# Kernel optimization log

Measured on AMD Instinct MI355X. Metric: run time of the kernel, lower is better.

The kernel has to match this reference:

```python
import jax, jax.numpy as jnp
import numpy as np

K_PRED = 6
SCORE_TEMPERATURE = 0.5
NMS_THRESH = np.array([2.5, 1.0, 1.5], dtype=np.float32)  # [veh, ped, cyc] meters
SUPPRESSED_SCORE = 0.001


def setup_inputs() -> dict:
    key = jax.random.key(0)
    k0, k1, k2, k3 = jax.random.split(key, 4)
    D, S, A, P, T = 1, 64, 128, 6, 80  # n_decoder, n_scene, n_agent, n_pred, n_step_future
    pred_valid = jnp.ones((S, A), dtype=bool)
    pred_conf = jax.random.normal(k0, (D, S, A, P), dtype=jnp.float32)
    # scale positions to realistic meters so distances straddle the NMS thresholds
    pred_pos = jax.random.normal(k1, (D, S, A, P, T, 2), dtype=jnp.float32) * 10.0
    pred_yaw_bbox = jax.random.normal(k2, (D, S, A, P, T, 1), dtype=jnp.float32)
    type_idx = jax.random.randint(k3, (S, A), 0, 3)
    ref_type = jax.nn.one_hot(type_idx, 3, dtype=jnp.float32)
    return {
        'pred_valid': pred_valid,
        'pred_conf': pred_conf,
        'pred_pos': pred_pos,
        'pred_yaw_bbox': pred_yaw_bbox,
        'ref_type': ref_type,
    }


def _nms_one_agent(scores, within, valid):
    # scores: [K], within: [K, K] bool, valid: scalar bool
    order = jnp.argsort(-scores)  # descending, computed once on original scores

    def step(cur, k):
        # suppress k if any other prediction within distance has a (currently) higher score
        mask = within[k] & (cur > cur[k])
        new_val = jnp.where(jnp.any(mask), jnp.asarray(SUPPRESSED_SCORE, cur.dtype), cur[k])
        return cur.at[k].set(new_val), None

    out, _ = jax.lax.scan(step, scores, order)
    return jnp.where(valid, out, scores)


_nms = jax.vmap(jax.vmap(_nms_one_agent))  # over scene, agent


def reference(pred_valid, pred_conf, pred_pos, pred_yaw_bbox, ref_type):
    D, S, A, P, T, _ = pred_pos.shape
    K = D * P
    # [n_scene, n_agent, k_pred, n_step, 2]
    trajs = jnp.moveaxis(pred_pos, 0, 2).reshape(S, A, K, T, 2)
    scores = jax.nn.softmax(pred_conf, axis=-1)
    scores = jnp.moveaxis(scores, 0, 2).reshape(S, A, K)
    scores = scores / jnp.sum(scores, axis=-1, keepdims=True)

    # mpa_nms: per-agent-type distance threshold
    thresh = jnp.einsum('sat,t->sa', ref_type, jnp.asarray(NMS_THRESH))[:, :, None, None]
    # use_ade=True: mean pairwise distance over time -> [S, A, K, K]
    diff = trajs[:, :, :, None] - trajs[:, :, None, :]          # [S,A,K,K,T,2]
    within_dist = jnp.mean(jnp.linalg.norm(diff, axis=-1), axis=-1) < thresh
    scores = _nms(scores, within_dist, pred_valid)
    scores = scores / jnp.sum(scores, axis=-1, keepdims=True)

    # score temperature
    scores = jax.nn.softmax(jnp.log(scores) / SCORE_TEMPERATURE, axis=-1)

    waymo_trajs = jnp.moveaxis(trajs, 3, 1)                      # [S, T, A, K, 2]
    waymo_scores = scores                                        # [S, A, K]
    waymo_valid = jnp.broadcast_to(pred_valid[:, None, :], (S, T, A))
    yaw_bbox = jnp.moveaxis(pred_yaw_bbox, 0, 2).reshape(S, A, K, T, 1)
    waymo_yaw_bbox = jnp.moveaxis(yaw_bbox, 3, 1)                # [S, T, A, K, 1]
    return waymo_valid, waymo_trajs, waymo_scores, waymo_yaw_bbox
```

## Files before the change

### kernel.cpp

```cpp
#include <hip/hip_runtime.h>
#include <hip/hip_bf16.h>

#define NS 64
#define NA 128
#define NK 6
#define NT 80
#define TILE_A 8
#define THREADS 256

#define OFF_TRAJ   655360
#define OFF_SCORE  (655360 + 7864320)
#define OFF_YAW    (655360 + 7864320 + 49152)

__global__ __launch_bounds__(THREADS) void waymo_post_kernel(
    const int*    __restrict__ validIn,
    const float*  __restrict__ confIn,
    const float2* __restrict__ posIn,
    const float*  __restrict__ yawIn,
    const float*  __restrict__ typeIn,
    float*        __restrict__ out)
{
    const int s   = blockIdx.y;
    const int a0  = blockIdx.x * TILE_A;
    const int tid = threadIdx.x;

    __shared__ float2 sPos[TILE_A * NK * 81];
    __shared__ float  sYaw[TILE_A * NK * 81];

    const size_t base = ((size_t)(s * NA + a0)) * NK * NT;
    for (int i = tid; i < TILE_A * NK * NT; i += THREADS) {
        int r = i / NT;
        int t = i - r * NT;
        sPos[r * 81 + t] = posIn[base + i];
        sYaw[r * 81 + t] = yawIn[base + i];
    }
    __syncthreads();

    float*  outV  = out;
    float2* outT  = (float2*)(out + OFF_TRAJ);
    float*  outSc = out + OFF_SCORE;
    float*  outY  = out + OFF_YAW;

    {
        const int la   = tid >> 5;
        const int lane = tid & 31;
        const int a    = a0 + la;
        const int p    = lane >> 1;
        const int half = lane & 1;

        const size_t sa = (size_t)s * NA + a;
        const float th = 2.5f * typeIn[sa * 3 + 0]
                       + 1.0f * typeIn[sa * 3 + 1]
                       + 1.5f * typeIn[sa * 3 + 2];

        int pi, pj;
        if      (p < 5)  { pi = 0; pj = p + 1; }
        else if (p < 9)  { pi = 1; pj = p - 3; }
        else if (p < 12) { pi = 2; pj = p - 6; }
        else if (p < 14) { pi = 3; pj = p - 8; }
        else             { pi = 4; pj = 5;     }

        const int rI = la * NK + pi, rJ = la * NK + pj;
        float dsum = 0.f;
        for (int t = half * 40; t < half * 40 + 40; ++t) {
            float2 u = sPos[rI * 81 + t];
            float2 v = sPos[rJ * 81 + t];
            float dx = u.x - v.x, dy = u.y - v.y;
            dsum += sqrtf(dx * dx + dy * dy);
        }
        dsum += __shfl_xor(dsum, 1);
        const bool within = (dsum / 80.0f) < th;
        const bool predb  = (half == 0) && (p < 15) && within;
        unsigned long long bal = __ballot(predb);
        unsigned mask32 = (unsigned)(bal >> (tid & 32));

        if (lane == 0) {
            float c[NK];
            float mx = -3e38f;
            for (int q = 0; q < NK; ++q) { c[q] = confIn[sa * NK + q]; mx = fmaxf(mx, c[q]); }
            float ssum = 0.f;
            for (int q = 0; q < NK; ++q) { c[q] = expf(c[q] - mx); ssum += c[q]; }
            for (int q = 0; q < NK; ++q) c[q] /= ssum;
            ssum = 0.f;
            for (int q = 0; q < NK; ++q) ssum += c[q];
            for (int q = 0; q < NK; ++q) c[q] /= ssum;

            int ord[NK]; bool used[NK];
            for (int q = 0; q < NK; ++q) used[q] = false;
            for (int st = 0; st < NK; ++st) {
                int best = 0; float bv = -3e38f;
                for (int q = 0; q < NK; ++q)
                    if (!used[q] && c[q] > bv) { bv = c[q]; best = q; }
                used[best] = true; ord[st] = best;
            }

            float cur[NK];
            for (int q = 0; q < NK; ++q) cur[q] = c[q];

            if (validIn[sa] != 0) {
                for (int st = 0; st < NK; ++st) {
                    int k = ord[st];
                    float ck = cur[k];
                    bool any = false;
                    for (int j = 0; j < NK; ++j) {
                        if (j == k) continue;
                        int lo = j < k ? j : k;
                        int hi = j < k ? k : j;
                        int pidx = lo * 5 - (lo * (lo - 1)) / 2 + (hi - lo - 1);
                        if (((mask32 >> (2 * pidx)) & 1u) && (cur[j] > ck)) any = true;
                    }
                    if (any) cur[k] = 0.001f;
                }
            }

            float tsum = 0.f;
            for (int q = 0; q < NK; ++q) tsum += cur[q];
            float w[NK]; float wsum = 0.f;
            for (int q = 0; q < NK; ++q) {
                float qq = cur[q] / tsum;
                w[q] = qq * qq; wsum += w[q];
            }
            for (int q = 0; q < NK; ++q) outSc[sa * NK + q] = w[q] / wsum;
        }
    }

    for (int o = tid; o < TILE_A * NK * NT; o += THREADS) {
        int t  = o / (TILE_A * NK);
        int r  = o - t * (TILE_A * NK);
        int la = r / NK;
        int k  = r - la * NK;
        size_t oidx = ((size_t)(s * NT + t) * NA + (a0 + la)) * NK + k;
        outT[oidx] = sPos[r * 81 + t];
        outY[oidx] = sYaw[r * 81 + t];
    }

    for (int o = tid; o < NT * TILE_A; o += THREADS) {
        int t  = o >> 3;
        int la = o & 7;
        outV[(size_t)(s * NT + t) * NA + a0 + la] =
            (validIn[(size_t)s * NA + a0 + la] != 0) ? 1.0f : 0.0f;
    }
}

extern "C" void kernel_launch(void* const* d_in, const int* in_sizes, int n_in,
                              void* d_out, int out_size, void* d_ws, size_t ws_size,
                              hipStream_t stream) {
    const int*    validIn = (const int*)d_in[0];
    const float*  confIn  = (const float*)d_in[1];
    const float2* posIn   = (const float2*)d_in[2];
    const float*  yawIn   = (const float*)d_in[3];
    const float*  typeIn  = (const float*)d_in[4];
    float* out = (float*)d_out;

    dim3 grid(NA / TILE_A, NS);
    waymo_post_kernel<<<grid, THREADS, 0, stream>>>(validIn, confIn, posIn, yawIn, typeIn, out);
}
```

Before: 42.50 us.

## Split into register-shuffle transpose kernel and separate NMS scoring kernel

```diff
diff --git a/kernel.cpp b/kernel.cpp
--- a/kernel.cpp
+++ b/kernel.cpp
@@ -5,140 +5,202 @@
 #define NA 128
 #define NK 6
 #define NT 80
-#define TILE_A 8
-#define THREADS 256
 
 #define OFF_TRAJ   655360
 #define OFF_SCORE  (655360 + 7864320)
 #define OFF_YAW    (655360 + 7864320 + 49152)
 
-__global__ __launch_bounds__(THREADS) void waymo_post_kernel(
+typedef float nfloat4 __attribute__((ext_vector_type(4)));
+
+__global__ __launch_bounds__(256) void k_move(
+    const int*    __restrict__ validIn,
+    const float2* __restrict__ posIn,
+    const float*  __restrict__ yawIn,
+    float*        __restrict__ out)
+{
+    const int bid  = blockIdx.x;
+    const int tid  = threadIdx.x;
+    const int lane = tid & 63;
+
+    if (bid < 768) {
+        const int wj = bid * 4 + (tid >> 6);
+        const int s  = wj / 48, rb = wj - s * 48;
+        const int r  = lane >> 2;
+        const int f  = lane & 3;
+
+        const nfloat4* in4  = (const nfloat4*)posIn;
+        nfloat4*       out4 = (nfloat4*)(out + OFF_TRAJ);
+
+        size_t ib = (size_t)(s * 768 + rb * 16 + r) * 40 + f;
+        size_t ob = (size_t)(s * 80 + 2 * f + (r & 1)) * 384 + rb * 8 + (r >> 1);
+
+        #pragma unroll
+        for (int it = 0; it < 10; ++it) {
+            nfloat4 v = in4[ib + it * 4];
+            nfloat4 x;
+            x.x = __shfl_xor(v.x, 4);
+            x.y = __shfl_xor(v.y, 4);
+            x.z = __shfl_xor(v.z, 4);
+            x.w = __shfl_xor(v.w, 4);
+            nfloat4 w;
+            if (r & 1) { w.x = x.z; w.y = x.w; w.z = v.z; w.w = v.w; }
+            else       { w.x = v.x; w.y = v.y; w.z = x.x; w.w = x.y; }
+            out4[ob + (size_t)it * 8 * 384] = w;
+        }
+    } else if (bid < 1536) {
+        const int wj = (bid - 768) * 4 + (tid >> 6);
+        const int s  = wj / 48, rb = wj - s * 48;
+        const int r  = lane & 15;
+        const int c  = lane >> 4;
+
+        const nfloat4* in4  = (const nfloat4*)yawIn;
+        nfloat4*       out4 = (nfloat4*)(out + OFF_YAW);
+
+        size_t ib = (size_t)(s * 768 + rb * 16 + r) * 20 + c;
+        size_t ob = (size_t)(s * 80 + c * 4 + (r & 3)) * 192 + rb * 4 + (r >> 2);
+
+        #pragma unroll
+        for (int tb = 0; tb < 5; ++tb) {
+            nfloat4 v = in4[ib + tb * 4];
+            nfloat4 a;
+            a.x = __shfl_xor(v.x, 1); a.y = __shfl_xor(v.y, 1);
+            a.z = __shfl_xor(v.z, 1); a.w = __shfl_xor(v.w, 1);
+            nfloat4 u;
+            if (r & 1) { u.x = a.y; u.y = v.y; u.z = a.w; u.w = v.w; }
+            else       { u.x = v.x; u.y = a.x; u.z = v.z; u.w = a.z; }
+            nfloat4 b;
+            b.x = __shfl_xor(u.x, 2); b.y = __shfl_xor(u.y, 2);
+            b.z = __shfl_xor(u.z, 2); b.w = __shfl_xor(u.w, 2);
+            nfloat4 o;
+            if (r & 2) { o.x = b.z; o.y = b.w; o.z = u.z; o.w = u.w; }
+            else       { o.x = u.x; o.y = u.y; o.z = b.x; o.w = b.y; }
+            out4[ob + (size_t)tb * 16 * 192] = o;
+        }
+    } else {
+        const int s = bid - 1536;
+        __shared__ nfloat4 vrow[NA / 4];
+        if (tid < 32) {
+            const int bse = s * NA + 4 * tid;
+            nfloat4 v;
+            v.x = (validIn[bse + 0] != 0) ? 1.0f : 0.0f;
+            v.y = (validIn[bse + 1] != 0) ? 1.0f : 0.0f;
+            v.z = (validIn[bse + 2] != 0) ? 1.0f : 0.0f;
+            v.w = (validIn[bse + 3] != 0) ? 1.0f : 0.0f;
+            vrow[tid] = v;
+        }
+        __syncthreads();
+        nfloat4* vOut = (nfloat4*)out;
+        for (int o = tid; o < NT * 32; o += 256) {
+            int t = o >> 5, q = o & 31;
+            vOut[(size_t)(s * NT + t) * 32 + q] = vrow[q];
+        }
+    }
+}
+
+#define SPS 82
+
+__global__ __launch_bounds__(256) void k_score(
     const int*    __restrict__ validIn,
     const float*  __restrict__ confIn,
     const float2* __restrict__ posIn,
-    const float*  __restrict__ yawIn,
     const float*  __restrict__ typeIn,
     float*        __restrict__ out)
 {
-    const int s   = blockIdx.y;
-    const int a0  = blockIdx.x * TILE_A;
+    const int g   = blockIdx.x;
     const int tid = threadIdx.x;
-
-    __shared__ float2 sPos[TILE_A * NK * 81];
-    __shared__ float  sYaw[TILE_A * NK * 81];
-
-    const size_t base = ((size_t)(s * NA + a0)) * NK * NT;
-    for (int i = tid; i < TILE_A * NK * NT; i += THREADS) {
-        int r = i / NT;
-        int t = i - r * NT;
-        sPos[r * 81 + t] = posIn[base + i];
-        sYaw[r * 81 + t] = yawIn[base + i];
+    const int s   = g >> 4;
+    const int a0  = (g & 15) * 8;
+
+    __shared__ float2 sPos[48 * SPS];
+
+    const float2* pbase = posIn + ((size_t)s * NA + a0) * (NK * NT);
+
+    for (int i = tid; i < 1920; i += 256) {
+        int r = i / 40, q = i - r * 40;
+        nfloat4 v = *(const nfloat4*)(pbase + (size_t)r * NT + 2 * q);
+        *(nfloat4*)&sPos[r * SPS + 2 * q] = v;
     }
     __syncthreads();
 
-    float*  outV  = out;
-    float2* outT  = (float2*)(out + OFF_TRAJ);
-    float*  outSc = out + OFF_SCORE;
-    float*  outY  = out + OFF_YAW;
-
-    {
-        const int la   = tid >> 5;
-        const int lane = tid & 31;
-        const int a    = a0 + la;
-        const int p    = lane >> 1;
-        const int half = lane & 1;
-
-        const size_t sa = (size_t)s * NA + a;
-        const float th = 2.5f * typeIn[sa * 3 + 0]
-                       + 1.0f * typeIn[sa * 3 + 1]
-                       + 1.5f * typeIn[sa * 3 + 2];
-
-        int pi, pj;
-        if      (p < 5)  { pi = 0; pj = p + 1; }
-        else if (p < 9)  { pi = 1; pj = p - 3; }
-        else if (p < 12) { pi = 2; pj = p - 6; }
-        else if (p < 14) { pi = 3; pj = p - 8; }
-        else             { pi = 4; pj = 5;     }
-
-        const int rI = la * NK + pi, rJ = la * NK + pj;
-        float dsum = 0.f;
-        for (int t = half * 40; t < half * 40 + 40; ++t) {
-            float2 u = sPos[rI * 81 + t];
-            float2 v = sPos[rJ * 81 + t];
-            float dx = u.x - v.x, dy = u.y - v.y;
-            dsum += sqrtf(dx * dx + dy * dy);
-        }
-        dsum += __shfl_xor(dsum, 1);
-        const bool within = (dsum / 80.0f) < th;
-        const bool predb  = (half == 0) && (p < 15) && within;
-        unsigned long long bal = __ballot(predb);
-        unsigned mask32 = (unsigned)(bal >> (tid & 32));
-
-        if (lane == 0) {
-            float c[NK];
-            float mx = -3e38f;
-            for (int q = 0; q < NK; ++q) { c[q] = confIn[sa * NK + q]; mx = fmaxf(mx, c[q]); }
-            float ssum = 0.f;
-            for (int q = 0; q < NK; ++q) { c[q] = expf(c[q] - mx); ssum += c[q]; }
-            for (int q = 0; q < NK; ++q) c[q] /= ssum;
-            ssum = 0.f;
-            for (int q = 0; q < NK; ++q) ssum += c[q];
-            for (int q = 0; q < NK; ++q) c[q] /= ssum;
-
-            int ord[NK]; bool used[NK];
-            for (int q = 0; q < NK; ++q) used[q] = false;
+    const int la   = tid >> 5;
+    const int lane = tid & 31;
+    const int p    = lane >> 1;
+    const int half = lane & 1;
+
+    const size_t sa = (size_t)s * NA + a0 + la;
+    const float th = 2.5f * typeIn[sa * 3 + 0]
+                   + 1.0f * typeIn[sa * 3 + 1]
+                   + 1.5f * typeIn[sa * 3 + 2];
+
+    int pi, pj;
+    if      (p < 5)  { pi = 0; pj = p + 1; }
+    else if (p < 9)  { pi = 1; pj = p - 3; }
+    else if (p < 12) { pi = 2; pj = p - 6; }
+    else if (p < 14) { pi = 3; pj = p - 8; }
+    else             { pi = 4; pj = 5;     }
+
+    const int rI = la * NK + pi, rJ = la * NK + pj;
+    float dsum = 0.f;
+    for (int t = half * 40; t < half * 40 + 40; ++t) {
+        float2 u = sPos[rI * SPS + t];
+        float2 v = sPos[rJ * SPS + t];
+        float dx = u.x - v.x, dy = u.y - v.y;
+        dsum += sqrtf(dx * dx + dy * dy);
+    }
+    dsum += __shfl_xor(dsum, 1);
+    const bool within = (dsum / 80.0f) < th;
+    const bool predb  = (half == 0) && (p < 15) && within;
+    unsigned long long bal = __ballot(predb);
+    unsigned mask32 = (unsigned)(bal >> (tid & 32));
+
+    if (lane == 0) {
+        float c[NK];
+        float mx = -3e38f;
+        for (int q = 0; q < NK; ++q) { c[q] = confIn[sa * NK + q]; mx = fmaxf(mx, c[q]); }
+        float ssum = 0.f;
+        for (int q = 0; q < NK; ++q) { c[q] = expf(c[q] - mx); ssum += c[q]; }
+        for (int q = 0; q < NK; ++q) c[q] /= ssum;
+        ssum = 0.f;
+        for (int q = 0; q < NK; ++q) ssum += c[q];
+        for (int q = 0; q < NK; ++q) c[q] /= ssum;
+
+        int ord[NK]; bool used[NK];
+        for (int q = 0; q < NK; ++q) used[q] = false;
+        for (int st = 0; st < NK; ++st) {
+            int best = 0; float bv = -3e38f;
+            for (int q = 0; q < NK; ++q)
+                if (!used[q] && c[q] > bv) { bv = c[q]; best = q; }
+            used[best] = true; ord[st] = best;
+        }
+
+        float cur[NK];
+        for (int q = 0; q < NK; ++q) cur[q] = c[q];
+
+        if (validIn[sa] != 0) {
             for (int st = 0; st < NK; ++st) {
-                int best = 0; float bv = -3e38f;
-                for (int q = 0; q < NK; ++q)
-                    if (!used[q] && c[q] > bv) { bv = c[q]; best = q; }
-                used[best] = true; ord[st] = best;
+                int k = ord[st];
+                float ck = cur[k];
+                bool any = false;
+                for (int j = 0; j < NK; ++j) {
+                    if (j == k) continue;
+                    int lo = j < k ? j : k;
+                    int hi = j < k ? k : j;
+                    int pidx = lo * 5 - (lo * (lo - 1)) / 2 + (hi - lo - 1);
+                    if (((mask32 >> (2 * pidx)) & 1u) && (cur[j] > ck)) any = true;
+                }
+                if (any) cur[k] = 0.001f;
             }
-
-            float cur[NK];
-            for (int q = 0; q < NK; ++q) cur[q] = c[q];
-
-            if (validIn[sa] != 0) {
-                for (int st = 0; st < NK; ++st) {
-                    int k = ord[st];
-                    float ck = cur[k];
-                    bool any = false;
-                    for (int j = 0; j < NK; ++j) {
-                        if (j == k) continue;
-                        int lo = j < k ? j : k;
-                        int hi = j < k ? k : j;
-                        int pidx = lo * 5 - (lo * (lo - 1)) / 2 + (hi - lo - 1);
-                        if (((mask32 >> (2 * pidx)) & 1u) && (cur[j] > ck)) any = true;
-                    }
-                    if (any) cur[k] = 0.001f;
-                }
-            }
-
-            float tsum = 0.f;
-            for (int q = 0; q < NK; ++q) tsum += cur[q];
-            float w[NK]; float wsum = 0.f;
-            for (int q = 0; q < NK; ++q) {
-                float qq = cur[q] / tsum;
-                w[q] = qq * qq; wsum += w[q];
-            }
-            for (int q = 0; q < NK; ++q) outSc[sa * NK + q] = w[q] / wsum;
-        }
-    }
-
-    for (int o = tid; o < TILE_A * NK * NT; o += THREADS) {
-        int t  = o / (TILE_A * NK);
-        int r  = o - t * (TILE_A * NK);
-        int la = r / NK;
-        int k  = r - la * NK;
-        size_t oidx = ((size_t)(s * NT + t) * NA + (a0 + la)) * NK + k;
-        outT[oidx] = sPos[r * 81 + t];
-        outY[oidx] = sYaw[r * 81 + t];
-    }
-
-    for (int o = tid; o < NT * TILE_A; o += THREADS) {
-        int t  = o >> 3;
-        int la = o & 7;
-        outV[(size_t)(s * NT + t) * NA + a0 + la] =
-            (validIn[(size_t)s * NA + a0 + la] != 0) ? 1.0f : 0.0f;
+        }
+
+        float tsum = 0.f;
+        for (int q = 0; q < NK; ++q) tsum += cur[q];
+        float w[NK]; float wsum = 0.f;
+        for (int q = 0; q < NK; ++q) {
+            float qq = cur[q] / tsum;
+            w[q] = qq * qq; wsum += w[q];
+        }
+        float* outSc = out + OFF_SCORE;
+        for (int q = 0; q < NK; ++q) outSc[sa * NK + q] = w[q] / wsum;
     }
 }
 
@@ -152,6 +214,6 @@
     const float*  typeIn  = (const float*)d_in[4];
     float* out = (float*)d_out;
 
-    dim3 grid(NA / TILE_A, NS);
-    waymo_post_kernel<<<grid, THREADS, 0, stream>>>(validIn, confIn, posIn, yawIn, typeIn, out);
+    k_move<<<1600, 256, 0, stream>>>(validIn, posIn, yawIn, out);
+    k_score<<<1024, 256, 0, stream>>>(validIn, confIn, posIn, typeIn, out);
 }
```

New measurement: 44.37 us. +4.4%, slower.
